# Kernel tuning notes

Hardware: AMD Instinct MI355X
Metric: run time of the kernel (lower is better)

The kernel has to match this reference:

```python
import jax, jax.numpy as jnp
import numpy as np

N_T, N_Q = 32768, 4096
E_T, E_Q = 1048576, 131072
H = 128
VOCAB = 1001  # num_features + 1
NUM_LAYERS = 3


def _sage_conv(x, edge_index, Wl, bl, Wr):
    # PyG SAGEConv, aggr='mean': out = lin_l(mean_j x_j) + lin_r(x_i)
    src, dst = edge_index[0], edge_index[1]
    n = x.shape[0]
    agg = jax.ops.segment_sum(x[src], dst, num_segments=n)          # [n, H]
    cnt = jax.ops.segment_sum(jnp.ones((src.shape[0],), x.dtype), dst, num_segments=n)
    mean = agg / jnp.maximum(cnt, 1.0)[:, None]
    return mean @ Wl.T + bl + x @ Wr.T


def setup_inputs() -> dict:
    key = jax.random.key(0)
    ks = jax.random.split(key, 12)
    target_x = jax.random.randint(ks[0], (N_T,), 0, VOCAB, dtype=jnp.int64 if jax.config.jax_enable_x64 else jnp.int32)
    query_x = jax.random.randint(ks[1], (N_Q,), 0, VOCAB, dtype=target_x.dtype)
    target_edge_index = jax.random.randint(ks[2], (2, E_T), 0, N_T, dtype=target_x.dtype)
    query_edge_index = jax.random.randint(ks[3], (2, E_Q), 0, N_Q, dtype=target_x.dtype)
    mask = jax.random.bernoulli(ks[4], 0.5, (N_Q, N_T))
    emb = jax.random.normal(ks[5], (VOCAB, H), jnp.float32) * 0.02
    s = 1.0 / np.sqrt(H)
    Wl = jax.random.uniform(ks[6], (NUM_LAYERS, H, H), jnp.float32, -s, s)
    bl = jax.random.uniform(ks[7], (NUM_LAYERS, H), jnp.float32, -s, s)
    Wr = jax.random.uniform(ks[8], (NUM_LAYERS, H, H), jnp.float32, -s, s)
    return {"target_x": target_x, "query_x": query_x,
            "target_edge_index": target_edge_index, "query_edge_index": query_edge_index,
            "mask": mask, "emb": emb, "Wl": Wl, "bl": bl, "Wr": Wr}


def reference(target_x, query_x, target_edge_index, query_edge_index, mask, emb, Wl, bl, Wr):
    et = emb[target_x]  # [N_T, H]
    eq = emb[query_x]   # [N_Q, H]
    for i in range(NUM_LAYERS):
        et = jax.nn.elu(_sage_conv(et, target_edge_index, Wl[i], bl[i], Wr[i]))
        eq = jax.nn.elu(_sage_conv(eq, query_edge_index, Wl[i], bl[i], Wr[i]))
    fmask = mask.astype(jnp.float32)
    att = (eq @ et.T) * fmask / jnp.sqrt(jnp.float32(H)) + (-1e9) * (1.0 - fmask)
    att = jax.nn.softmax(att, axis=1)
    return att[None]  # [1, N_Q, N_T]
```

## Files before the change

kernel.cpp:

```cpp
#include <hip/hip_runtime.h>
#include <stdint.h>

#define N_T 32768
#define N_Q 4096
#define E_T 1048576
#define E_Q 131072
#define H   128
#define NL  3
#define VOCAB 1001

typedef float    f32x4 __attribute__((ext_vector_type(4)));
typedef int      i32x4 __attribute__((ext_vector_type(4)));
typedef _Float16 f16x8 __attribute__((ext_vector_type(8)));

__device__ __forceinline__ ushort f2h(float x){
  union{_Float16 h; ushort u;} c; c.h = (_Float16)x; return c.u;
}
__device__ __forceinline__ float h2f(unsigned u){
  union{ushort u; _Float16 h;} c; c.u = (ushort)u; return (float)c.h;
}

__global__ void setup_k(int* cnt_t, int* cnt_q, float* rowsum, int* flag,
                        const unsigned* m){
  int b = blockIdx.x, t = threadIdx.x;
  if(b < 128){ cnt_t[b*256+t] = 0; }
  else if(b < 144){ cnt_q[(b-128)*256+t] = 0; }
  else if(b < 160){ rowsum[(b-144)*256+t] = 0.f; }
  else {
    if(t == 0) *flag = 0;
    __syncthreads();
    int f = 0;
    for(int j=t;j<4096;j+=256){
      unsigned v = m[j];
      if(v > 1u) f |= (v & 0xFEFEFEFEu) ? 2 : 1;
    }
    if(f) atomicOr(flag, f);
  }
}

__global__ void cvt_k(const float* __restrict__ Wl, const float* __restrict__ Wr,
                      ushort* __restrict__ WH, ushort* __restrict__ WLo,
                      const float* __restrict__ emb, ushort* __restrict__ emb16){
  int b = blockIdx.x, t = threadIdx.x;
  if(b < 96){
    int i = b*256 + t;
    int k  = (i & 63) * 4;
    int c  = (i >> 6) & 127;
    int l  = i >> 13;
    const float* src = (k < 128)
        ? &Wl[((size_t)l*128 + c)*128 + k]
        : &Wr[((size_t)l*128 + c)*128 + (k-128)];
    float4 v = *(const float4*)src;
    ushort4 h, lo;
    h.x = f2h(v.x); lo.x = f2h(v.x - h2f(h.x));
    h.y = f2h(v.y); lo.y = f2h(v.y - h2f(h.y));
    h.z = f2h(v.z); lo.z = f2h(v.z - h2f(h.z));
    h.w = f2h(v.w); lo.w = f2h(v.w - h2f(h.w));
    size_t off = ((size_t)l*128 + c)*256 + k;
    *(ushort4*)&WH[off]  = h;
    *(ushort4*)&WLo[off] = lo;
  } else {
    int i = (b-96)*256 + t;
    if(i >= VOCAB*H/8) return;
    float4 v0 = ((const float4*)emb)[(size_t)i*2];
    float4 v1 = ((const float4*)emb)[(size_t)i*2 + 1];
    uint4 u;
    u.x = (unsigned)f2h(v0.x) | ((unsigned)f2h(v0.y)<<16);
    u.y = (unsigned)f2h(v0.z) | ((unsigned)f2h(v0.w)<<16);
    u.z = (unsigned)f2h(v1.x) | ((unsigned)f2h(v1.y)<<16);
    u.w = (unsigned)f2h(v1.z) | ((unsigned)f2h(v1.w)<<16);
    ((uint4*)emb16)[i] = u;
  }
}

__global__ void count2_k(const int* __restrict__ te, const int* __restrict__ qe,
                         int* cnt_t, int* cnt_q){
  int b = blockIdx.x;
  if(b < E_T/256){
    int i = b*256 + threadIdx.x;
    atomicAdd(&cnt_t[te[E_T + i]], 1);
  } else {
    int i = (b - E_T/256)*256 + threadIdx.x;
    atomicAdd(&cnt_q[qe[E_Q + i]], 1);
  }
}

__device__ __forceinline__ void scan_body(const int* cnt, int n, int* rp, int* pos){
  __shared__ int part[1024];
  int t = threadIdx.x;
  int chunk = (n + 1023) >> 10;
  int lo = t*chunk, hi = lo+chunk; if(hi>n) hi=n;
  int s = 0;
  for(int i=lo;i<hi;i++) s += cnt[i];
  part[t] = s;
  __syncthreads();
  for(int off=1; off<1024; off<<=1){
    int v = (t >= off) ? part[t-off] : 0;
    __syncthreads();
    part[t] += v;
    __syncthreads();
  }
  int run = (t==0) ? 0 : part[t-1];
  for(int i=lo;i<hi;i++){ rp[i]=run; pos[i]=run; run += cnt[i]; }
  if(t==0) rp[n] = part[1023];
}

__global__ void scan2_k(const int* cnt_t, int* rp_t, int* pos_t,
                        const int* cnt_q, int* rp_q, int* pos_q){
  if(blockIdx.x == 0) scan_body(cnt_t, N_T, rp_t, pos_t);
  else                scan_body(cnt_q, N_Q, rp_q, pos_q);
}

__global__ void fill2_k(const int* __restrict__ te, const int* __restrict__ qe,
                        int* pos_t, int* csr_t, int* pos_q, int* csr_q){
  int b = blockIdx.x;
  if(b < E_T/256){
    int i = b*256 + threadIdx.x;
    int p = atomicAdd(&pos_t[te[E_T + i]], 1);
    csr_t[p] = te[i];
  } else {
    int i = (b - E_T/256)*256 + threadIdx.x;
    int p = atomicAdd(&pos_q[qe[E_Q + i]], 1);
    csr_q[p] = qe[i];
  }
}

__device__ __forceinline__ void agg_body(const ushort* x, const int* nid,
    const ushort* emb16, const int* rp, const int* csr, ushort* agg,
    int wid, int lane){
  const unsigned* xw = (const unsigned*)x;
  const unsigned* ew = (const unsigned*)emb16;
  int rs = rp[wid], re = rp[wid+1];
  float px[8], py[8];
  #pragma unroll
  for(int q=0;q<8;q++){ px[q]=0.f; py[q]=0.f; }
  int j = rs;
  if(nid){
    for(; j+8 <= re; j+=8){
      #pragma unroll
      for(int q=0;q<8;q++){
        unsigned u = ew[(size_t)nid[csr[j+q]]*64 + lane];
        px[q] += h2f(u & 0xFFFFu); py[q] += h2f(u >> 16);
      }
    }
    for(; j < re; j++){
      unsigned u = ew[(size_t)nid[csr[j]]*64 + lane];
      px[0] += h2f(u & 0xFFFFu); py[0] += h2f(u >> 16);
    }
  } else {
    for(; j+8 <= re; j+=8){
      #pragma unroll
      for(int q=0;q<8;q++){
        unsigned u = xw[(size_t)csr[j+q]*64 + lane];
        px[q] += h2f(u & 0xFFFFu); py[q] += h2f(u >> 16);
      }
    }
    for(; j < re; j++){
      unsigned u = xw[(size_t)csr[j]*64 + lane];
      px[0] += h2f(u & 0xFFFFu); py[0] += h2f(u >> 16);
    }
  }
  float sx = ((px[0]+px[1]) + (px[2]+px[3])) + ((px[4]+px[5]) + (px[6]+px[7]));
  float sy = ((py[0]+py[1]) + (py[2]+py[3])) + ((py[4]+py[5]) + (py[6]+py[7]));
  int c = re - rs; if(c < 1) c = 1;
  float inv = 1.0f / (float)c;
  ((unsigned*)agg)[(size_t)wid*64 + lane] =
      (unsigned)f2h(sx*inv) | ((unsigned)f2h(sy*inv) << 16);
}

__global__ void agg2_k(const ushort* xt, const ushort* xq,
                       const int* nidt, const int* nidq, const ushort* emb16,
                       const int* rp_t, const int* csr_t,
                       const int* rp_q, const int* csr_q,
                       ushort* aggt, ushort* aggq){
  int b = blockIdx.x;
  int lane = threadIdx.x & 63;
  int wv = threadIdx.x >> 6;
  if(b < N_T/4){
    agg_body(xt, nidt, emb16, rp_t, csr_t, aggt, b*4 + wv, lane);
  } else {
    agg_body(xq, nidq, emb16, rp_q, csr_q, aggq, (b - N_T/4)*4 + wv, lane);
  }
}

__global__ __launch_bounds__(256,3) void layer2_k(
    const ushort* __restrict__ aggT, const ushort* __restrict__ xT,
    const int* __restrict__ nidT, ushort* __restrict__ outT,
    const ushort* __restrict__ aggQ, const ushort* __restrict__ xQ,
    const int* __restrict__ nidQ, ushort* __restrict__ outQ,
    const ushort* __restrict__ emb16,
    const ushort* __restrict__ WH, const ushort* __restrict__ WLo,
    const float* __restrict__ bl){
  __shared__ ushort SM3[3*128*64];
  ushort* SA = SM3;
  ushort* SH = SM3 + 8192;
  ushort* SL = SM3 + 16384;
  int bq = (int)blockIdx.x - (N_T/128);
  const ushort* agg   = (bq < 0) ? aggT : aggQ;
  const ushort* xprev = (bq < 0) ? xT   : xQ;
  const int*    nid   = (bq < 0) ? nidT : nidQ;
  ushort*       out16 = (bq < 0) ? outT : outQ;
  int r0g = ((bq < 0) ? (int)blockIdx.x : bq) * 128;
  int t = threadIdx.x;
  int lane = t & 63;
  int w = t >> 6;
  int wr = w >> 1, wc = w & 1;
  int fr = lane & 15, kg0 = lane >> 4;
  f32x4 acc[4][4] = {};
  for(int kt=0; kt<4; kt++){
    __syncthreads();
    int ko = (kt & 1) * 64;
    #pragma unroll
    for(int it=0; it<4; it++){
      int idx = t + it*256;
      int row = idx >> 3, k8 = idx & 7;
      int sw = (k8 ^ (row & 7)) * 8;
      uint4 av;
      if(kt < 2){
        av = *(const uint4*)&agg[(size_t)(r0g+row)*H + ko + k8*8];
      } else if(nid){
        av = *(const uint4*)&emb16[(size_t)nid[r0g+row]*H + ko + k8*8];
      } else {
        av = *(const uint4*)&xprev[(size_t)(r0g+row)*H + ko + k8*8];
      }
      *(uint4*)&SA[row*64 + sw] = av;
      *(uint4*)&SH[row*64 + sw] = *(const uint4*)&WH[row*256 + kt*64 + k8*8];
      *(uint4*)&SL[row*64 + sw] = *(const uint4*)&WLo[row*256 + kt*64 + k8*8];
    }
    __syncthreads();
    #pragma unroll
    for(int s=0; s<2; s++){
      int kg = s*4 + kg0;
      f16x8 a[4], bh[4], blo[4];
      #pragma unroll
      for(int m=0;m<4;m++){
        int ar = wr*64 + m*16 + fr;
        a[m] = *(const f16x8*)&SA[ar*64 + ((kg ^ (ar & 7)) << 3)];
      }
      #pragma unroll
      for(int n=0;n<4;n++){
        int bc = wc*64 + n*16 + fr;
        int ib = bc*64 + ((kg ^ (bc & 7)) << 3);
        bh[n]  = *(const f16x8*)&SH[ib];
        blo[n] = *(const f16x8*)&SL[ib];
      }
      #pragma unroll
      for(int m=0;m<4;m++)
        #pragma unroll
        for(int n=0;n<4;n++){
          acc[m][n] = __builtin_amdgcn_mfma_f32_16x16x32_f16(a[m], bh[n],  acc[m][n], 0,0,0);
          acc[m][n] = __builtin_amdgcn_mfma_f32_16x16x32_f16(a[m], blo[n], acc[m][n], 0,0,0);
        }
    }
  }
  __syncthreads();
  ushort* LT = SM3;
  #pragma unroll
  for(int n=0;n<4;n++){
    int c = wc*64 + n*16 + fr;
    float b = bl[c];
    #pragma unroll
    for(int m=0;m<4;m++){
      int r = wr*64 + m*16 + kg0*4;
      #pragma unroll
      for(int reg=0;reg<4;reg++){
        float v = acc[m][n][reg] + b;
        v = (v > 0.f) ? v : expm1f(v);
        LT[(r+reg)*128 + c] = f2h(v);
      }
    }
  }
  __syncthreads();
  #pragma unroll
  for(int i=0;i<8;i++){
    int idx = t + i*256;
    int row = idx >> 4, c8 = idx & 15;
    *(uint4*)&out16[(size_t)(r0g+row)*H + c8*8] = *(uint4*)&LT[row*128 + c8*8];
  }
}

__device__ __forceinline__ unsigned nib8(unsigned x, unsigned y){
  unsigned r = (x & 0xFu) | ((x>>4)&0xF0u) | ((x>>8)&0xF00u) | ((x>>12)&0xF000u);
  unsigned s = (y & 0xFu) | ((y>>4)&0xF0u) | ((y>>8)&0xF00u) | ((y>>12)&0xF000u);
  return r | (s<<16);
}
__device__ __forceinline__ unsigned pk4(unsigned u){
  return ((u & 0xFFu)       ? 1u : 0u) | ((u & 0xFF00u)     ? 2u : 0u)
       | ((u & 0xFF0000u)   ? 4u : 0u) | ((u & 0xFF000000u) ? 8u : 0u);
}

__device__ __forceinline__ void stage_mask_tile(const void* maskp, int mb,
    int gr0, int gc0, unsigned* MB, uint8_t* NB, unsigned* bitsOut, int t){
  if(mb & 2){
    const f32x4* base = (const f32x4*)maskp;
    #pragma unroll
    for(int i=0;i<16;i++){
      int idx = i*256 + t;
      int row = idx >> 5, c4 = idx & 31;
      f32x4 v = __builtin_nontemporal_load(
          &base[((size_t)(gr0+row)*N_T + gc0) / 4 + c4]);
      NB[row*32 + c4] = (uint8_t)((unsigned)(v[0]!=0.f) | ((unsigned)(v[1]!=0.f)<<1)
                                | ((unsigned)(v[2]!=0.f)<<2) | ((unsigned)(v[3]!=0.f)<<3));
    }
  } else if(mb & 1){
    const uint8_t* base = (const uint8_t*)maskp;
    #pragma unroll
    for(int i=0;i<16;i++){
      int idx = i*256 + t;
      int row = idx >> 5, c4 = idx & 31;
      unsigned u = __builtin_nontemporal_load(
          (const unsigned*)&base[(size_t)(gr0+row)*N_T + gc0 + c4*4]);
      NB[row*32 + c4] = (uint8_t)pk4(u);
    }
  } else {
    const i32x4* base = (const i32x4*)maskp;
    #pragma unroll
    for(int i=0;i<16;i++){
      int idx = i*256 + t;
      int row = idx >> 5, c4 = idx & 31;
      i32x4 v = __builtin_nontemporal_load(
          &base[((size_t)(gr0+row)*N_T + gc0) / 4 + c4]);
      NB[row*32 + c4] = (uint8_t)((unsigned)(v[0]!=0) | ((unsigned)(v[1]!=0)<<1)
                                | ((unsigned)(v[2]!=0)<<2) | ((unsigned)(v[3]!=0)<<3));
    }
  }
  __syncthreads();
  if(t < 128){
    uint4 a = *(const uint4*)&NB[t*32];
    uint4 b = *(const uint4*)&NB[t*32 + 16];
    unsigned w0 = nib8(a.x, a.y), w1 = nib8(a.z, a.w);
    unsigned w2 = nib8(b.x, b.y), w3 = nib8(b.z, b.w);
    MB[t*4]   = w0; MB[t*4+1] = w1;
    MB[t*4+2] = w2; MB[t*4+3] = w3;
    if(bitsOut){
      uint4 o; o.x=w0; o.y=w1; o.z=w2; o.w=w3;
      *(uint4*)&bitsOut[(size_t)(gr0 + t)*(N_T/32) + (gc0 >> 5)] = o;
    }
  }
}

__device__ __forceinline__ void att_tile(int bid, int& gc0, int& gr0){
  int xcd = bid & 7;
  int idx = bid >> 3;
  gc0 = (xcd*32 + (idx & 31)) * 128;
  gr0 = (idx >> 5) * 128;
}

__device__ __forceinline__ void qk_gemm(
    const ushort* __restrict__ A16, const ushort* __restrict__ B16,
    int abase, int bbase, int t, ushort* SM, f32x4 (&acc)[4][4]){
  ushort* AB = SM;
  ushort* BB = SM + 8192;
  int lane = t & 63;
  int w = t >> 6;
  int wr = w >> 1, wc = w & 1;
  int fr = lane & 15, kg0 = lane >> 4;
  for(int kt=0; kt<2; kt++){
    __syncthreads();
    #pragma unroll
    for(int it=0; it<4; it++){
      int idx = t + it*256;
      int row = idx >> 3, k8 = idx & 7;
      int sw = (k8 ^ (row & 7)) * 8;
      *(uint4*)&AB[row*64 + sw] = *(const uint4*)&A16[(size_t)(abase+row)*H + kt*64 + k8*8];
      *(uint4*)&BB[row*64 + sw] = *(const uint4*)&B16[(size_t)(bbase+row)*H + kt*64 + k8*8];
    }
    __syncthreads();
    #pragma unroll
    for(int s=0; s<2; s++){
      int kg = s*4 + kg0;
      f16x8 a[4], b[4];
      #pragma unroll
      for(int m=0;m<4;m++){
        int ar = wr*64 + m*16 + fr;
        a[m] = *(const f16x8*)&AB[ar*64 + ((kg ^ (ar & 7)) << 3)];
      }
      #pragma unroll
      for(int n=0;n<4;n++){
        int bc = wc*64 + n*16 + fr;
        b[n] = *(const f16x8*)&BB[bc*64 + ((kg ^ (bc & 7)) << 3)];
      }
      #pragma unroll
      for(int m=0;m<4;m++)
        #pragma unroll
        for(int n=0;n<4;n++)
          acc[m][n] = __builtin_amdgcn_mfma_f32_16x16x32_f16(a[m], b[n], acc[m][n], 0,0,0);
    }
  }
}

__global__ __launch_bounds__(256,4) void attsum_k(
    const ushort* __restrict__ eq16, const ushort* __restrict__ et16,
    const void* __restrict__ maskp, const int* __restrict__ flag,
    unsigned* __restrict__ bitsOut, float* __restrict__ rowsum){
  __shared__ ushort SM[2*128*64];
  __shared__ __align__(16) unsigned MB[512];
  __shared__ float RS[128][2];
  int t = threadIdx.x;
  int gc0, gr0;
  att_tile(blockIdx.x, gc0, gr0);
  int lane = t & 63;
  int w = t >> 6;
  int wr = w >> 1, wc = w & 1;
  int fr = lane & 15, kg0 = lane >> 4;

  int mb = *flag;
  stage_mask_tile(maskp, mb, gr0, gc0, MB, (uint8_t*)SM, bitsOut, t);

  f32x4 acc[4][4] = {};
  qk_gemm(et16, eq16, gc0, gr0, t, SM, acc);

  const float sc = 0.08838834764831845f;
  #pragma unroll
  for(int n=0;n<4;n++){
    int q = wc*64 + n*16 + fr;
    float s = 0.f;
    #pragma unroll
    for(int m=0;m<4;m++){
      unsigned wb = MB[q*4 + wr*2 + (m>>1)];
      int off = ((m&1)<<4) | (kg0<<2);
      s += ((wb>>(off+0))&1u) ? __expf(acc[m][n][0]*sc) : 0.f;
      s += ((wb>>(off+1))&1u) ? __expf(acc[m][n][1]*sc) : 0.f;
      s += ((wb>>(off+2))&1u) ? __expf(acc[m][n][2]*sc) : 0.f;
      s += ((wb>>(off+3))&1u) ? __expf(acc[m][n][3]*sc) : 0.f;
    }
    s += __shfl_xor(s, 16);
    s += __shfl_xor(s, 32);
    if(lane < 16) RS[q][wr] = s;
  }
  __syncthreads();
  if(t < 128) atomicAdd(&rowsum[gr0 + t], RS[t][0] + RS[t][1]);
}

__global__ __launch_bounds__(256,4) void attout_k(
    const ushort* __restrict__ eq16, const ushort* __restrict__ et16,
    const void* __restrict__ maskp, const int* __restrict__ flag,
    const unsigned* __restrict__ bitsIn, const float* __restrict__ rowsum,
    float* __restrict__ out){
  __shared__ ushort SM[2*128*64];
  __shared__ __align__(16) unsigned MB[512];
  __shared__ float IRS[128];
  int t = threadIdx.x;
  int gc0, gr0;
  att_tile(blockIdx.x, gc0, gr0);
  int lane = t & 63;
  int w = t >> 6;
  int wr = w >> 1, wc = w & 1;
  int fr = lane & 15, kg0 = lane >> 4;

  if(bitsIn){
    if(t < 128)
      *(uint4*)&MB[t*4] = *(const uint4*)&bitsIn[(size_t)(gr0 + t)*(N_T/32) + (gc0 >> 5)];
  } else {
    int mb = *flag;
    stage_mask_tile(maskp, mb, gr0, gc0, MB, (uint8_t*)SM, nullptr, t);
  }
  if(t < 128) IRS[t] = 1.0f / rowsum[gr0 + t];

  f32x4 acc[4][4] = {};
  qk_gemm(et16, eq16, gc0, gr0, t, SM, acc);

  const float sc = 0.08838834764831845f;
  #pragma unroll
  for(int n=0;n<4;n++){
    int q = wc*64 + n*16 + fr;
    float ir = IRS[q];
    size_t rb = (size_t)(gr0 + q)*N_T + gc0 + wr*64;
    #pragma unroll
    for(int m=0;m<4;m++){
      unsigned wb = MB[q*4 + wr*2 + (m>>1)];
      int off = ((m&1)<<4) | (kg0<<2);
      f32x4 o;
      o[0] = ((wb>>(off+0))&1u) ? __expf(acc[m][n][0]*sc)*ir : 0.f;
      o[1] = ((wb>>(off+1))&1u) ? __expf(acc[m][n][1]*sc)*ir : 0.f;
      o[2] = ((wb>>(off+2))&1u) ? __expf(acc[m][n][2]*sc)*ir : 0.f;
      o[3] = ((wb>>(off+3))&1u) ? __expf(acc[m][n][3]*sc)*ir : 0.f;
      __builtin_nontemporal_store(o, (f32x4*)&out[rb + m*16 + (kg0<<2)]);
    }
  }
}

extern "C" void kernel_launch(void* const* d_in, const int* in_sizes, int n_in,
                              void* d_out, int out_size, void* d_ws, size_t ws_size,
                              hipStream_t stream){
  const int* tx  = (const int*)d_in[0];
  const int* qx  = (const int*)d_in[1];
  const int* te  = (const int*)d_in[2];
  const int* qe  = (const int*)d_in[3];
  const void* mask = d_in[4];
  const float* emb = (const float*)d_in[5];
  const float* Wl  = (const float*)d_in[6];
  const float* bl  = (const float*)d_in[7];
  const float* Wr  = (const float*)d_in[8];
  float* out = (float*)d_out;

  ushort* et16 = (ushort*)d_ws;
  ushort* eq16 = et16 + (size_t)N_T*H;
  float* rowsum = (float*)((char*)d_ws + ((size_t)9 << 20));
  int*   flag   = (int*)(rowsum + N_Q);
  ushort* WH  = (ushort*)((char*)d_ws + ((size_t)10 << 20));
  ushort* WLo = WH + (size_t)NL*128*256;
  ushort* emb16 = (ushort*)((char*)d_ws + ((size_t)11 << 20));
  bool useBits = ws_size >= ((size_t)37 << 20);
  unsigned* bits = useBits ? (unsigned*)((char*)d_ws + ((size_t)19 << 20)) : nullptr;

  char* S = (char*)d_out;
  ushort* xt0  = (ushort*)(S);
  ushort* xt1  = (ushort*)(S + 8388608);
  ushort* aggt = (ushort*)(S + 16777216);
  ushort* xq0  = (ushort*)(S + 25165824);
  ushort* xq1  = (ushort*)(S + 26214400);
  ushort* aggq = (ushort*)(S + 27262976);
  int*   cnt_t = (int*)(S + 28311552);
  int*   rp_t  = cnt_t + N_T;
  int*   pos_t = rp_t + N_T + 1;
  int*   csr_t = pos_t + N_T;
  int*   cnt_q = csr_t + E_T;
  int*   rp_q  = cnt_q + N_Q;
  int*   pos_q = rp_q + N_Q + 1;
  int*   csr_q = pos_q + N_Q;

  setup_k<<<161,256,0,stream>>>(cnt_t, cnt_q, rowsum, flag, (const unsigned*)mask);
  cvt_k<<<159,256,0,stream>>>(Wl, Wr, WH, WLo, emb, emb16);
  count2_k<<<E_T/256 + E_Q/256,256,0,stream>>>(te, qe, cnt_t, cnt_q);
  scan2_k<<<2,1024,0,stream>>>(cnt_t, rp_t, pos_t, cnt_q, rp_q, pos_q);
  fill2_k<<<E_T/256 + E_Q/256,256,0,stream>>>(te, qe, pos_t, csr_t, pos_q, csr_q);

  ushort* outs_t[NL] = {xt0, xt1, et16};
  ushort* outs_q[NL] = {xq0, xq1, eq16};
  const ushort* cur_t = nullptr;
  const ushort* cur_q = nullptr;
  for(int l=0;l<NL;l++){
    const ushort* wh = WH  + (size_t)l*128*256;
    const ushort* wl = WLo + (size_t)l*128*256;
    const int* nidt = (l==0) ? tx : nullptr;
    const int* nidq = (l==0) ? qx : nullptr;
    agg2_k<<<N_T/4 + N_Q/4,256,0,stream>>>(cur_t, cur_q, nidt, nidq, emb16,
                                           rp_t, csr_t, rp_q, csr_q, aggt, aggq);
    layer2_k<<<N_T/128 + N_Q/128,256,0,stream>>>(aggt, cur_t, nidt, outs_t[l],
                                                 aggq, cur_q, nidq, outs_q[l],
                                                 emb16, wh, wl, bl+(size_t)l*H);
    cur_t = outs_t[l];
    cur_q = outs_q[l];
  }

  attsum_k<<<8192,256,0,stream>>>(eq16, et16, mask, flag, bits, rowsum);
  attout_k<<<8192,256,0,stream>>>(eq16, et16, mask, flag, bits, rowsum, out);
}
```

Before: 645.5 us.

## Bucket target CSR edges by source range and merge setup kernels

```diff
diff --git a/kernel.cpp b/kernel.cpp
--- a/kernel.cpp
+++ b/kernel.cpp
@@ -20,13 +20,16 @@
   union{ushort u; _Float16 h;} c; c.u = (ushort)u; return (float)c.h;
 }
 
-__global__ void setup_k(int* cnt_t, int* cnt_q, float* rowsum, int* flag,
-                        const unsigned* m){
+__global__ void init_k(int* cnt_t, int* cnt_q, float* rowsum, int* flag,
+                       const unsigned* m,
+                       const float* __restrict__ Wl, const float* __restrict__ Wr,
+                       ushort* __restrict__ WH, ushort* __restrict__ WLo,
+                       const float* __restrict__ emb, ushort* __restrict__ emb16){
   int b = blockIdx.x, t = threadIdx.x;
-  if(b < 128){ cnt_t[b*256+t] = 0; }
-  else if(b < 144){ cnt_q[(b-128)*256+t] = 0; }
-  else if(b < 160){ rowsum[(b-144)*256+t] = 0.f; }
-  else {
+  if(b < 512){ cnt_t[b*256+t] = 0; }
+  else if(b < 528){ cnt_q[(b-512)*256+t] = 0; }
+  else if(b < 544){ rowsum[(b-528)*256+t] = 0.f; }
+  else if(b == 544){
     if(t == 0) *flag = 0;
     __syncthreads();
     int f = 0;
@@ -36,14 +39,8 @@
     }
     if(f) atomicOr(flag, f);
   }
-}
-
-__global__ void cvt_k(const float* __restrict__ Wl, const float* __restrict__ Wr,
-                      ushort* __restrict__ WH, ushort* __restrict__ WLo,
-                      const float* __restrict__ emb, ushort* __restrict__ emb16){
-  int b = blockIdx.x, t = threadIdx.x;
-  if(b < 96){
-    int i = b*256 + t;
+  else if(b < 641){
+    int i = (b-545)*256 + t;
     int k  = (i & 63) * 4;
     int c  = (i >> 6) & 127;
     int l  = i >> 13;
@@ -60,7 +57,7 @@
     *(ushort4*)&WH[off]  = h;
     *(ushort4*)&WLo[off] = lo;
   } else {
-    int i = (b-96)*256 + t;
+    int i = (b-641)*256 + t;
     if(i >= VOCAB*H/8) return;
     float4 v0 = ((const float4*)emb)[(size_t)i*2];
     float4 v1 = ((const float4*)emb)[(size_t)i*2 + 1];
@@ -78,7 +75,8 @@
   int b = blockIdx.x;
   if(b < E_T/256){
     int i = b*256 + threadIdx.x;
-    atomicAdd(&cnt_t[te[E_T + i]], 1);
+    int dst = te[E_T + i], src = te[i];
+    atomicAdd(&cnt_t[(dst<<2) | (src>>13)], 1);
   } else {
     int i = (b - E_T/256)*256 + threadIdx.x;
     atomicAdd(&cnt_q[qe[E_Q + i]], 1);
@@ -91,7 +89,12 @@
   int chunk = (n + 1023) >> 10;
   int lo = t*chunk, hi = lo+chunk; if(hi>n) hi=n;
   int s = 0;
-  for(int i=lo;i<hi;i++) s += cnt[i];
+  int i = lo;
+  for(; i+4 <= hi; i+=4){
+    i32x4 v = *(const i32x4*)&cnt[i];
+    s += v[0]+v[1]+v[2]+v[3];
+  }
+  for(; i < hi; i++) s += cnt[i];
   part[t] = s;
   __syncthreads();
   for(int off=1; off<1024; off<<=1){
@@ -101,13 +104,21 @@
     __syncthreads();
   }
   int run = (t==0) ? 0 : part[t-1];
-  for(int i=lo;i<hi;i++){ rp[i]=run; pos[i]=run; run += cnt[i]; }
+  i = lo;
+  for(; i+4 <= hi; i+=4){
+    i32x4 v = *(const i32x4*)&cnt[i];
+    rp[i]=run;   pos[i]=run;   run += v[0];
+    rp[i+1]=run; pos[i+1]=run; run += v[1];
+    rp[i+2]=run; pos[i+2]=run; run += v[2];
+    rp[i+3]=run; pos[i+3]=run; run += v[3];
+  }
+  for(; i < hi; i++){ rp[i]=run; pos[i]=run; run += cnt[i]; }
   if(t==0) rp[n] = part[1023];
 }
 
 __global__ void scan2_k(const int* cnt_t, int* rp_t, int* pos_t,
                         const int* cnt_q, int* rp_q, int* pos_q){
-  if(blockIdx.x == 0) scan_body(cnt_t, N_T, rp_t, pos_t);
+  if(blockIdx.x == 0) scan_body(cnt_t, 4*N_T, rp_t, pos_t);
   else                scan_body(cnt_q, N_Q, rp_q, pos_q);
 }
 
@@ -116,8 +127,9 @@
   int b = blockIdx.x;
   if(b < E_T/256){
     int i = b*256 + threadIdx.x;
-    int p = atomicAdd(&pos_t[te[E_T + i]], 1);
-    csr_t[p] = te[i];
+    int dst = te[E_T + i], src = te[i];
+    int p = atomicAdd(&pos_t[(dst<<2) | (src>>13)], 1);
+    csr_t[p] = src;
   } else {
     int i = (b - E_T/256)*256 + threadIdx.x;
     int p = atomicAdd(&pos_q[qe[E_Q + i]], 1);
@@ -126,11 +138,10 @@
 }
 
 __device__ __forceinline__ void agg_body(const ushort* x, const int* nid,
-    const ushort* emb16, const int* rp, const int* csr, ushort* agg,
-    int wid, int lane){
+    const ushort* emb16, const int* csr, ushort* agg,
+    int wid, int rs, int re, int lane){
   const unsigned* xw = (const unsigned*)x;
   const unsigned* ew = (const unsigned*)emb16;
-  int rs = rp[wid], re = rp[wid+1];
   float px[8], py[8];
   #pragma unroll
   for(int q=0;q<8;q++){ px[q]=0.f; py[q]=0.f; }
@@ -170,16 +181,18 @@
 
 __global__ void agg2_k(const ushort* xt, const ushort* xq,
                        const int* nidt, const int* nidq, const ushort* emb16,
-                       const int* rp_t, const int* csr_t,
-                       const int* rp_q, const int* csr_q,
+                       const int* __restrict__ rp_t, const int* __restrict__ csr_t,
+                       const int* __restrict__ rp_q, const int* __restrict__ csr_q,
                        ushort* aggt, ushort* aggq){
   int b = blockIdx.x;
   int lane = threadIdx.x & 63;
   int wv = threadIdx.x >> 6;
   if(b < N_T/4){
-    agg_body(xt, nidt, emb16, rp_t, csr_t, aggt, b*4 + wv, lane);
-  } else {
-    agg_body(xq, nidq, emb16, rp_q, csr_q, aggq, (b - N_T/4)*4 + wv, lane);
+    int wid = b*4 + wv;
+    agg_body(xt, nidt, emb16, csr_t, aggt, wid, rp_t[wid*4], rp_t[wid*4+4], lane);
+  } else {
+    int wid = (b - N_T/4)*4 + wv;
+    agg_body(xq, nidq, emb16, csr_q, aggq, wid, rp_q[wid], rp_q[wid+1], lane);
   }
 }
 
@@ -512,16 +525,16 @@
   ushort* xq1  = (ushort*)(S + 26214400);
   ushort* aggq = (ushort*)(S + 27262976);
   int*   cnt_t = (int*)(S + 28311552);
-  int*   rp_t  = cnt_t + N_T;
-  int*   pos_t = rp_t + N_T + 1;
-  int*   csr_t = pos_t + N_T;
+  int*   rp_t  = cnt_t + 4*N_T;
+  int*   pos_t = rp_t + 4*N_T + 1;
+  int*   csr_t = pos_t + 4*N_T;
   int*   cnt_q = csr_t + E_T;
   int*   rp_q  = cnt_q + N_Q;
   int*   pos_q = rp_q + N_Q + 1;
   int*   csr_q = pos_q + N_Q;
 
-  setup_k<<<161,256,0,stream>>>(cnt_t, cnt_q, rowsum, flag, (const unsigned*)mask);
-  cvt_k<<<159,256,0,stream>>>(Wl, Wr, WH, WLo, emb, emb16);
+  init_k<<<704,256,0,stream>>>(cnt_t, cnt_q, rowsum, flag, (const unsigned*)mask,
+                               Wl, Wr, WH, WLo, emb, emb16);
   count2_k<<<E_T/256 + E_Q/256,256,0,stream>>>(te, qe, cnt_t, cnt_q);
   scan2_k<<<2,1024,0,stream>>>(cnt_t, rp_t, pos_t, cnt_q, rp_q, pos_q);
   fill2_k<<<E_T/256 + E_Q/256,256,0,stream>>>(te, qe, pos_t, csr_t, pos_q, csr_q);
```

Measured after the change: 764.7 us. +18.5%, slower.
